# Performance work log

Hardware: AMD Instinct MI355X
Metric: run time of the kernel (lower is better)

## Reference

```python
import jax, jax.numpy as jnp
import numpy as np

LOG2PI = float(np.log(2.0 * np.pi))


def setup_inputs() -> dict:
    key = jax.random.key(0)
    ks = jax.random.split(key, 5)
    B, T, XD, C = 128, 2050, 6, 64
    return {
        "x": jax.random.normal(ks[0], (B, T, XD), jnp.float32),
        "observation_means": jax.random.uniform(ks[1], (C, XD), dtype=jnp.float32),
        "observation_stddevs": jax.random.uniform(ks[2], (C, XD), dtype=jnp.float32),
        "log_A": jax.random.normal(ks[3], (C, C), jnp.float32),
        "log_pi": jax.random.normal(ks[4], (C,), jnp.float32),
    }


def _emission_logprob(x, means, stds):
    # Normal(means[:, :4], relu(stds[:, :4]) + 0.1).log_prob(x[:, :, :4]) summed over feat dim
    mu = means[:, :4]                       # (C,4)
    sigma = jax.nn.relu(stds[:, :4]) + 0.1  # (C,4)
    z = (x[:, :, None, :4] - mu) / sigma    # (B,T,C,4)
    return jnp.sum(-0.5 * z * z - jnp.log(sigma) - 0.5 * LOG2PI, axis=-1)  # (B,T,C)


def _forward_scalers(logp, log_A, log_pi):
    # scaled HMM forward pass; returns per-step log normalizers (T,B)
    a0 = logp[:, 0] + log_pi
    s0 = jax.nn.logsumexp(a0, axis=-1)
    a0n = a0 - s0[:, None]

    def step(a_prev, lp_t):
        a = lp_t + jax.nn.logsumexp(a_prev[:, :, None] + log_A[None], axis=1)
        s = jax.nn.logsumexp(a, axis=-1)
        return a - s[:, None], s

    _, s_rest = jax.lax.scan(step, a0n, jnp.swapaxes(logp[:, 1:], 0, 1))
    return jnp.concatenate([s0[None], s_rest], axis=0)  # (T,B)


def _viterbi(logp, log_A, log_pi):
    d0 = logp[:, 0] + log_pi  # (B,C)

    def step(d_prev, lp_t):
        scores = d_prev[:, :, None] + log_A[None]  # (B,C_prev,C_cur)
        psi_t = jnp.argmax(scores, axis=1)
        d = jnp.max(scores, axis=1) + lp_t
        return d, psi_t

    d_last, psi = jax.lax.scan(step, d0, jnp.swapaxes(logp[:, 1:], 0, 1))  # psi: (T-1,B,C)
    c_last = jnp.argmax(d_last, axis=-1)  # (B,)

    def back(c_next, psi_t):
        c_t = jnp.take_along_axis(psi_t, c_next[:, None], axis=1)[:, 0]
        return c_t, c_t

    _, cs = jax.lax.scan(back, c_last, psi, reverse=True)  # (T-1,B)
    c = jnp.concatenate([cs, c_last[None]], axis=0)  # (T,B)
    return jnp.swapaxes(c, 0, 1)  # (B,T)


def reference(x, observation_means, observation_stddevs, log_A, log_pi):
    logA = jax.nn.log_softmax(log_A, axis=1)
    logpi = jax.nn.log_softmax(log_pi, axis=0)
    logp = _emission_logprob(x, observation_means, observation_stddevs)  # (B,T,C)
    scalers = _forward_scalers(logp, logA, logpi)                         # (T,B)
    logp_x = jnp.sum(scalers, axis=0)                                     # (B,)
    c_est = _viterbi(logp, logA, logpi)                                   # (B,T) int
    return logp_x, c_est
```

## Files before the change

### kernel.cpp

```cpp
#include <hip/hip_runtime.h>

#define T_LEN 2050
#define B_SZ 128
#define NCHUNK 33
#define HL2PI 0.91893853320467274178f

__device__ __forceinline__ float waveMax(float v) {
#pragma unroll
    for (int off = 32; off >= 1; off >>= 1)
        v = fmaxf(v, __shfl_xor(v, off, 64));
    return v;
}
__device__ __forceinline__ float waveSum(float v) {
#pragma unroll
    for (int off = 32; off >= 1; off >>= 1)
        v += __shfl_xor(v, off, 64);
    return v;
}
__device__ __forceinline__ void waveArgmax(float& v, int& idx) {
#pragma unroll
    for (int off = 32; off >= 1; off >>= 1) {
        float ov = __shfl_xor(v, off, 64);
        int   oi = __shfl_xor(idx, off, 64);
        if (ov > v || (ov == v && oi < idx)) { v = ov; idx = oi; }
    }
}
__device__ __forceinline__ void cfence() { asm volatile("" ::: "memory"); }

__device__ __forceinline__ float rl(float v, int lane) {
    return __int_as_float(__builtin_amdgcn_readlane(__float_as_int(v), lane));
}

__device__ __forceinline__ float dppSumAll(float v) {
#define SSTEP(ctrl) { int t_ = __builtin_amdgcn_update_dpp(0, __float_as_int(v), ctrl, 0xf, 0xf, true); \
                      v = v + __int_as_float(t_); }
    SSTEP(0x111) SSTEP(0x112) SSTEP(0x114) SSTEP(0x118) SSTEP(0x142) SSTEP(0x143)
#undef SSTEP
    return __int_as_float(__builtin_amdgcn_readlane(__float_as_int(v), 63));
}
__device__ __forceinline__ float dppMaxAll(float v) {
#define MSTEP(ctrl) { int t_ = __builtin_amdgcn_update_dpp(__float_as_int(v), __float_as_int(v), ctrl, 0xf, 0xf, false); \
                      v = fmaxf(v, __int_as_float(t_)); }
    MSTEP(0x111) MSTEP(0x112) MSTEP(0x114) MSTEP(0x118) MSTEP(0x142) MSTEP(0x143)
#undef MSTEP
    return __int_as_float(__builtin_amdgcn_readlane(__float_as_int(v), 63));
}

extern "C" __global__ __launch_bounds__(64, 1)
void hmm_prep(const float* __restrict__ logA_in,
              const float* __restrict__ logpi_in,
              float* __restrict__ lAg,
              float* __restrict__ lpig)
{
    __shared__ float la[64 * 65];
    __shared__ float rowlse[64];
    const int j = threadIdx.x;
#pragma unroll
    for (int k = 0; k < 64; ++k)
        la[k * 65 + j] = logA_in[k * 64 + j];
    cfence();
    {
        float m = -1e30f;
#pragma unroll
        for (int k = 0; k < 64; ++k) m = fmaxf(m, la[j * 65 + k]);
        float s = 0.f;
#pragma unroll
        for (int k = 0; k < 64; ++k) s += expf(la[j * 65 + k] - m);
        rowlse[j] = m + logf(s);
    }
    cfence();
    {
        float v = logpi_in[j];
        float m = waveMax(v);
        float s = waveSum(expf(v - m));
        lpig[j] = v - (m + logf(s));
    }
    float4* o = (float4*)lAg;
#pragma unroll
    for (int k = 0; k < 16; ++k) {
        float4 v;
        v.x = la[(4 * k + 0) * 65 + j] - rowlse[4 * k + 0];
        v.y = la[(4 * k + 1) * 65 + j] - rowlse[4 * k + 1];
        v.z = la[(4 * k + 2) * 65 + j] - rowlse[4 * k + 2];
        v.w = la[(4 * k + 3) * 65 + j] - rowlse[4 * k + 3];
        o[j * 16 + k] = v;
    }
}

extern "C" __global__ __launch_bounds__(256)
void hmm_emis(const float* __restrict__ x,
              const float* __restrict__ means,
              const float* __restrict__ stds,
              float* __restrict__ buf,
              float* __restrict__ m_pre)
{
    const int wid = blockIdx.x * 4 + (threadIdx.x >> 6);
    const int j = threadIdx.x & 63;
    const int t = wid >> 7;
    const int b = wid & 127;

    const float* xt = x + ((size_t)b * T_LEN + t) * 6;
    float x0 = xt[0], x1 = xt[1], x2 = xt[2], x3 = xt[3];

    float mu0 = means[j * 6 + 0], mu1 = means[j * 6 + 1];
    float mu2 = means[j * 6 + 2], mu3 = means[j * 6 + 3];
    float sg0 = fmaxf(stds[j * 6 + 0], 0.f) + 0.1f;
    float sg1 = fmaxf(stds[j * 6 + 1], 0.f) + 0.1f;
    float sg2 = fmaxf(stds[j * 6 + 2], 0.f) + 0.1f;
    float sg3 = fmaxf(stds[j * 6 + 3], 0.f) + 0.1f;
    float ls0 = logf(sg0), ls1 = logf(sg1), ls2 = logf(sg2), ls3 = logf(sg3);

    float z0 = (x0 - mu0) / sg0, z1 = (x1 - mu1) / sg1;
    float z2 = (x2 - mu2) / sg2, z3 = (x3 - mu3) / sg3;
    float e0 = ((-0.5f * z0) * z0 - ls0) - HL2PI;
    float e1 = ((-0.5f * z1) * z1 - ls1) - HL2PI;
    float e2 = ((-0.5f * z2) * z2 - ls2) - HL2PI;
    float e3 = ((-0.5f * z3) * z3 - ls3) - HL2PI;
    float lp = ((e0 + e1) + e2) + e3;

    buf[((size_t)b * T_LEN + t) * 64 + j] = lp;
    float mm = waveMax(lp);
    if (j == 0) m_pre[(size_t)b * T_LEN + t] = mm;
}

#define VIT_REDUCE(SRC)                                                   \
    float m0 = -3.4e38f, m1 = -3.4e38f, m2 = -3.4e38f, m3 = -3.4e38f;     \
    _Pragma("unroll")                                                     \
    for (int gq = 0; gq < 4; ++gq) {                                      \
        float s_[16];                                                     \
        _Pragma("unroll")                                                 \
        for (int m_ = 0; m_ < 16; ++m_) s_[m_] = rl((SRC), 16 * gq + m_); \
        __builtin_amdgcn_sched_barrier(0);                                \
        _Pragma("unroll")                                                 \
        for (int k2 = 0; k2 < 4; k2 += 2) {                               \
            const int ia = 16 * gq + 4 * k2;                              \
            const int ib = ia + 4;                                        \
            float a0_ = s_[4*k2+0] + lA[ia+0], b0_ = s_[4*k2+4] + lA[ib+0]; \
            float a1_ = s_[4*k2+1] + lA[ia+1], b1_ = s_[4*k2+5] + lA[ib+1]; \
            float a2_ = s_[4*k2+2] + lA[ia+2], b2_ = s_[4*k2+6] + lA[ib+2]; \
            float a3_ = s_[4*k2+3] + lA[ia+3], b3_ = s_[4*k2+7] + lA[ib+3]; \
            m0 = fmaxf(fmaxf(m0, a0_), b0_);                              \
            m1 = fmaxf(fmaxf(m1, a1_), b1_);                              \
            m2 = fmaxf(fmaxf(m2, a2_), b2_);                              \
            m3 = fmaxf(fmaxf(m3, a3_), b3_);                              \
        }                                                                 \
    }

extern "C" __global__ __launch_bounds__(64, 1)
void hmm_main(const float* __restrict__ x,
              const float* __restrict__ means,
              const float* __restrict__ stds,
              const float* __restrict__ lAg,
              const float* __restrict__ lpig,
              float* __restrict__ out,
              float* __restrict__ buf,
              const float* __restrict__ m_pre,
              int* __restrict__ c_last)
{
    __shared__ __align__(16) float xs[12304];

    const int j   = threadIdx.x;
    const int bid = blockIdx.x;
    const bool is_fwd = (bid < B_SZ);
    const int b = is_fwd ? bid : bid - B_SZ;

    float lpi = lpig[j];

    if (is_fwd) {
        {
            const float4* xg4 = (const float4*)(x + (size_t)b * T_LEN * 6);
            float4* xs4 = (float4*)xs;
            for (int i = j; i < 3075; i += 64) xs4[i] = xg4[i];
        }
        float mu0 = means[j * 6 + 0], mu1 = means[j * 6 + 1];
        float mu2 = means[j * 6 + 2], mu3 = means[j * 6 + 3];
        float sg0 = fmaxf(stds[j * 6 + 0], 0.f) + 0.1f;
        float sg1 = fmaxf(stds[j * 6 + 1], 0.f) + 0.1f;
        float sg2 = fmaxf(stds[j * 6 + 2], 0.f) + 0.1f;
        float sg3 = fmaxf(stds[j * 6 + 3], 0.f) + 0.1f;
        float ls0 = logf(sg0), ls1 = logf(sg1), ls2 = logf(sg2), ls3 = logf(sg3);
        float i0 = 1.f / sg0, i1 = 1.f / sg1, i2 = 1.f / sg2, i3 = 1.f / sg3;
        float cst = -(ls0 + ls1 + ls2 + ls3) - 4.f * HL2PI;

        float Ac[64];
        {
            const float4* g = (const float4*)lAg;
#pragma unroll
            for (int k = 0; k < 16; ++k) {
                float4 v = g[j * 16 + k];
                Ac[4 * k + 0] = __expf(v.x); Ac[4 * k + 1] = __expf(v.y);
                Ac[4 * k + 2] = __expf(v.z); Ac[4 * k + 3] = __expf(v.w);
            }
        }
        cfence();

        float z0 = (xs[0] - mu0) * i0, z1 = (xs[1] - mu1) * i1;
        float z2 = (xs[2] - mu2) * i2, z3 = (xs[3] - mu3) * i3;
        float a0 = (cst - 0.5f * (z0 * z0 + z1 * z1 + z2 * z2 + z3 * z3)) + lpi;
        float m0a = dppMaxAll(a0);
        float u = __expf(a0 - m0a);
        float s0 = dppSumAll(u);
        double acc = (double)(m0a + __logf(s0));
        u *= (1.0f / s0);

        const float* mp = m_pre + (size_t)b * T_LEN;
        float g0 = mp[1], g1 = mp[2], g2 = mp[3], g3 = mp[4];

#pragma unroll 1
        for (int t = 1; t < T_LEN; ++t) {
            float mm_c = g0; g0 = g1; g1 = g2; g2 = g3;
            int tp = t + 4; if (tp > T_LEN - 1) tp = T_LEN - 1;
            g3 = mp[tp];

            int o = t * 6;
            float y0 = xs[o], y1 = xs[o + 1], y2 = xs[o + 2], y3 = xs[o + 3];
            float w0 = (y0 - mu0) * i0, w1 = (y1 - mu1) * i1;
            float w2 = (y2 - mu2) * i2, w3 = (y3 - mu3) * i3;
            float lp = cst - 0.5f * (w0 * w0 + w1 * w1 + w2 * w2 + w3 * w3);
            float e_c = __expf(lp - mm_c);

            float q0 = 0.f, q1 = 0.f, q2 = 0.f, q3 = 0.f;
#pragma unroll
            for (int gq = 0; gq < 4; ++gq) {
                float s[16];
#pragma unroll
                for (int m = 0; m < 16; ++m) s[m] = rl(u, 16 * gq + m);
#pragma unroll
                for (int k2 = 0; k2 < 4; ++k2) {
                    const int i = 16 * gq + 4 * k2;
                    q0 = fmaf(s[4 * k2 + 0], Ac[i + 0], q0);
                    q1 = fmaf(s[4 * k2 + 1], Ac[i + 1], q1);
                    q2 = fmaf(s[4 * k2 + 2], Ac[i + 2], q2);
                    q3 = fmaf(s[4 * k2 + 3], Ac[i + 3], q3);
                }
            }
            u = ((q0 + q1) + (q2 + q3)) * e_c;
            acc += (double)mm_c;
            if ((t & 3) == 0) {
                float ss = dppSumAll(u);
                acc += (double)__logf(ss);
                u *= (1.0f / ss);
            }
        }
        float sf = dppSumAll(u);
        acc += (double)__logf(sf);
        if (j == 0) out[b] = (float)acc;
    } else {
        float lA[64];
        {
            const float4* g = (const float4*)lAg;
#pragma unroll
            for (int k = 0; k < 16; ++k) {
                float4 v = g[j * 16 + k];
                lA[4 * k + 0] = v.x; lA[4 * k + 1] = v.y;
                lA[4 * k + 2] = v.z; lA[4 * k + 3] = v.w;
            }
        }
        float* bb = buf + (size_t)b * T_LEN * 64 + j;

        float dn = bb[0] + lpi;
        float lr[8];
#pragma unroll
        for (int i = 0; i < 8; ++i) lr[i] = bb[(size_t)(1 + i) * 64];
        bb[0] = dn;

#pragma unroll 1
        for (int tb = 1; tb <= 2033; tb += 8) {
#pragma unroll
            for (int q = 0; q < 8; ++q) {
                const int t = tb + q;
                float lp_c = lr[q];
                lr[q] = bb[(size_t)(t + 8) * 64];
                VIT_REDUCE(dn);
                dn = fmaxf(fmaxf(m0, m1), fmaxf(m2, m3)) + lp_c;
                bb[(size_t)t * 64] = dn;
            }
        }
        float l_last = bb[(size_t)2049 * 64];
#pragma unroll
        for (int q = 0; q < 8; ++q) {
            const int t = 2041 + q;
            float lp_c = lr[q];
            VIT_REDUCE(dn);
            dn = fmaxf(fmaxf(m0, m1), fmaxf(m2, m3)) + lp_c;
            bb[(size_t)t * 64] = dn;
        }
        {
            float lp_c = l_last;
            VIT_REDUCE(dn);
            dn = fmaxf(fmaxf(m0, m1), fmaxf(m2, m3)) + lp_c;
        }

        float vv = dn; int idx = j;
        waveArgmax(vv, idx);
        if (j == 0) c_last[b] = idx;
    }
}

extern "C" __global__ __launch_bounds__(256)
void hmm_psi(const float* __restrict__ buf,
             const float* __restrict__ lAg,
             unsigned char* __restrict__ psi)
{
    __shared__ __align__(16) float sd[4][64];
    const int warp = threadIdx.x >> 6;
    const int j = threadIdx.x & 63;
    const int wid = blockIdx.x * 4 + warp;

    float lA[64];
    {
        const float4* g = (const float4*)lAg;
#pragma unroll
        for (int k = 0; k < 16; ++k) {
            float4 v = g[j * 16 + k];
            lA[4 * k + 0] = v.x; lA[4 * k + 1] = v.y;
            lA[4 * k + 2] = v.z; lA[4 * k + 3] = v.w;
        }
    }
    const float4* dv = (const float4*)sd[warp];
    const int NP = 2049 * B_SZ;

    for (int p = wid; p < NP; p += 8192) {
        const int t = (p >> 7) + 1;
        const int b = p & 127;
        float dval = buf[((size_t)b * T_LEN + (t - 1)) * 64 + j];
        sd[warp][j] = dval;

        float bv0 = -3.4e38f, bv1 = -3.4e38f, bv2 = -3.4e38f, bv3 = -3.4e38f;
        int bi0 = 0, bi1 = 1, bi2 = 2, bi3 = 3;
#pragma unroll
        for (int k = 0; k < 16; ++k) {
            float4 dd = dv[k];
            float v0 = dd.x + lA[4 * k + 0];
            float v1 = dd.y + lA[4 * k + 1];
            float v2 = dd.z + lA[4 * k + 2];
            float v3 = dd.w + lA[4 * k + 3];
            if (v0 > bv0) { bv0 = v0; bi0 = 4 * k + 0; }
            if (v1 > bv1) { bv1 = v1; bi1 = 4 * k + 1; }
            if (v2 > bv2) { bv2 = v2; bi2 = 4 * k + 2; }
            if (v3 > bv3) { bv3 = v3; bi3 = 4 * k + 3; }
        }
        float best = bv0; int bidx = bi0;
        if (bv1 > best || (bv1 == best && bi1 < bidx)) { best = bv1; bidx = bi1; }
        if (bv2 > best || (bv2 == best && bi2 < bidx)) { best = bv2; bidx = bi2; }
        if (bv3 > best || (bv3 == best && bi3 < bidx)) { best = bv3; bidx = bi3; }

        psi[((size_t)t * B_SZ + b) * 64 + j] = (unsigned char)bidx;
    }
}

extern "C" __global__ __launch_bounds__(256)
void hmm_compose(const unsigned char* __restrict__ psi,
                 unsigned char* __restrict__ mt)
{
    const int w = blockIdx.x * 4 + (threadIdx.x >> 6);
    const int j = threadIdx.x & 63;
    const int g = w % NCHUNK;
    const int b = w / NCHUNK;
    const int e  = (g < NCHUNK - 1) ? g * 64 + 64 : (T_LEN - 1);
    const int t0 = g * 64 + 1;

    int M = j;
    int r[8];
#pragma unroll
    for (int i = 0; i < 8; ++i) {
        int t = e - i;
        r[i] = (t >= t0) ? (int)psi[((size_t)t * B_SZ + b) * 64 + j] : 0;
    }
#pragma unroll 1
    for (int t = e; t >= t0; --t) {
        const int q = (e - t) & 7;
        int row = r[q];
        int tn = t - 8;
        r[q] = (tn >= t0) ? (int)psi[((size_t)tn * B_SZ + b) * 64 + j] : 0;
        M = __builtin_amdgcn_ds_bpermute(M << 2, row);
    }
    mt[((size_t)g * B_SZ + b) * 64 + j] = (unsigned char)M;
}

extern "C" __global__ __launch_bounds__(64, 1)
void hmm_bound(const unsigned char* __restrict__ mt,
               const int* __restrict__ c_last,
               int* __restrict__ sbg)
{
    const int b = blockIdx.x;
    const int j = threadIdx.x;
    int rows[NCHUNK];
#pragma unroll
    for (int q = 0; q < NCHUNK; ++q)
        rows[q] = (int)mt[((size_t)q * B_SZ + b) * 64 + j];
    int cur = c_last[b];
#pragma unroll
    for (int q = NCHUNK - 1; q >= 0; --q) {
        cur = __builtin_amdgcn_readlane(rows[q], cur);
        if (j == 0) sbg[b * NCHUNK + q] = cur;
    }
}

extern "C" __global__ __launch_bounds__(256)
void hmm_fill(const unsigned char* __restrict__ psi,
              const int* __restrict__ sbg,
              const int* __restrict__ c_last,
              float* __restrict__ out)
{
    const int w = blockIdx.x * 4 + (threadIdx.x >> 6);
    const int j = threadIdx.x & 63;
    const int g = w % NCHUNK;
    const int b = w / NCHUNK;
    const int cl = c_last[b];
    float* oc = out + B_SZ + (size_t)b * T_LEN;

    const int e  = (g < NCHUNK - 1) ? g * 64 + 64 : (T_LEN - 1);
    const int t0 = g * 64 + 1;
    int s = (g < NCHUNK - 1) ? sbg[b * NCHUNK + g + 1] : cl;
    if (g == NCHUNK - 1 && j == 0) oc[T_LEN - 1] = (float)cl;

    int r[8];
#pragma unroll
    for (int i = 0; i < 8; ++i) {
        int t = e - i;
        r[i] = (t >= t0) ? (int)psi[((size_t)t * B_SZ + b) * 64 + j] : 0;
    }
#pragma unroll 1
    for (int t = e; t >= t0; --t) {
        const int q = (e - t) & 7;
        int row = r[q];
        int tn = t - 8;
        r[q] = (tn >= t0) ? (int)psi[((size_t)tn * B_SZ + b) * 64 + j] : 0;
        s = __builtin_amdgcn_readlane(row, s);
        if (j == 0) oc[t - 1] = (float)s;
    }
}

extern "C" void kernel_launch(void* const* d_in, const int* in_sizes, int n_in,
                              void* d_out, int out_size, void* d_ws, size_t ws_size,
                              hipStream_t stream)
{
    const float* x      = (const float*)d_in[0];
    const float* means  = (const float*)d_in[1];
    const float* stds   = (const float*)d_in[2];
    const float* logA   = (const float*)d_in[3];
    const float* logpi  = (const float*)d_in[4];
    float* out = (float*)d_out;

    char* base = (char*)d_ws;
    float*         buf   = (float*)base;
    unsigned char* psi   = (unsigned char*)(base + 67174400);
    float*         m_pre = (float*)(base + 67174400);
    unsigned char* mt    = (unsigned char*)(base + 83968000);
    int*           cl    = (int*)(base + 84238336);
    float*         lAg   = (float*)(base + 84238848);
    float*         lpig  = (float*)(base + 84255232);
    int*           sbg   = (int*)base;

    hipLaunchKernelGGL(hmm_prep, dim3(1), dim3(64), 0, stream, logA, logpi, lAg, lpig);
    hipLaunchKernelGGL(hmm_emis, dim3((T_LEN * B_SZ) / 4), dim3(256), 0, stream,
                       x, means, stds, buf, m_pre);
    hipLaunchKernelGGL(hmm_main, dim3(2 * B_SZ), dim3(64), 0, stream,
                       x, means, stds, lAg, lpig, out, buf, m_pre, cl);
    hipLaunchKernelGGL(hmm_psi, dim3(2048), dim3(256), 0, stream, buf, lAg, psi);
    hipLaunchKernelGGL(hmm_compose, dim3((NCHUNK * B_SZ) / 4), dim3(256), 0, stream, psi, mt);
    hipLaunchKernelGGL(hmm_bound, dim3(B_SZ), dim3(64), 0, stream, mt, cl, sbg);
    hipLaunchKernelGGL(hmm_fill, dim3((NCHUNK * B_SZ) / 4), dim3(256), 0, stream, psi, sbg, cl, out);
}
```

Measured before the change: 1.018 ms.

## Fuse prep into emission kernel and merge backtrace stages into cooperative kernel

Folds the logA/logpi normalisation into block 0 of the emission kernel, and merges the psi, compose, bound and fill kernels into one cooperative kernel with grid.sync between stages. The aim is to remove several kernel launches and their inter-launch gaps. In exchange, the psi stage now runs on 768 blocks instead of 2048, and cooperative launch plus grid-wide barriers add their own costs. Moving prep into emis is safe because emis does not read lAg and hmm_main runs after emis.

```diff
diff --git a/kernel.cpp b/kernel.cpp
--- a/kernel.cpp
+++ b/kernel.cpp
@@ -1,4 +1,7 @@
 #include <hip/hip_runtime.h>
+#include <hip/hip_cooperative_groups.h>
+
+namespace cg = cooperative_groups;
 
 #define T_LEN 2050
 #define B_SZ 128
@@ -46,54 +49,20 @@
     return __int_as_float(__builtin_amdgcn_readlane(__float_as_int(v), 63));
 }
 
-extern "C" __global__ __launch_bounds__(64, 1)
-void hmm_prep(const float* __restrict__ logA_in,
+extern "C" __global__ __launch_bounds__(256)
+void hmm_emis(const float* __restrict__ x,
+              const float* __restrict__ means,
+              const float* __restrict__ stds,
+              float* __restrict__ buf,
+              float* __restrict__ m_pre,
+              const float* __restrict__ logA_in,
               const float* __restrict__ logpi_in,
               float* __restrict__ lAg,
               float* __restrict__ lpig)
 {
     __shared__ float la[64 * 65];
     __shared__ float rowlse[64];
-    const int j = threadIdx.x;
-#pragma unroll
-    for (int k = 0; k < 64; ++k)
-        la[k * 65 + j] = logA_in[k * 64 + j];
-    cfence();
-    {
-        float m = -1e30f;
-#pragma unroll
-        for (int k = 0; k < 64; ++k) m = fmaxf(m, la[j * 65 + k]);
-        float s = 0.f;
-#pragma unroll
-        for (int k = 0; k < 64; ++k) s += expf(la[j * 65 + k] - m);
-        rowlse[j] = m + logf(s);
-    }
-    cfence();
-    {
-        float v = logpi_in[j];
-        float m = waveMax(v);
-        float s = waveSum(expf(v - m));
-        lpig[j] = v - (m + logf(s));
-    }
-    float4* o = (float4*)lAg;
-#pragma unroll
-    for (int k = 0; k < 16; ++k) {
-        float4 v;
-        v.x = la[(4 * k + 0) * 65 + j] - rowlse[4 * k + 0];
-        v.y = la[(4 * k + 1) * 65 + j] - rowlse[4 * k + 1];
-        v.z = la[(4 * k + 2) * 65 + j] - rowlse[4 * k + 2];
-        v.w = la[(4 * k + 3) * 65 + j] - rowlse[4 * k + 3];
-        o[j * 16 + k] = v;
-    }
-}
-
-extern "C" __global__ __launch_bounds__(256)
-void hmm_emis(const float* __restrict__ x,
-              const float* __restrict__ means,
-              const float* __restrict__ stds,
-              float* __restrict__ buf,
-              float* __restrict__ m_pre)
-{
+
     const int wid = blockIdx.x * 4 + (threadIdx.x >> 6);
     const int j = threadIdx.x & 63;
     const int t = wid >> 7;
@@ -121,6 +90,39 @@
     buf[((size_t)b * T_LEN + t) * 64 + j] = lp;
     float mm = waveMax(lp);
     if (j == 0) m_pre[(size_t)b * T_LEN + t] = mm;
+
+    if (blockIdx.x == 0 && threadIdx.x < 64) {
+#pragma unroll
+        for (int k = 0; k < 64; ++k)
+            la[k * 65 + j] = logA_in[k * 64 + j];
+        cfence();
+        {
+            float m = -1e30f;
+#pragma unroll
+            for (int k = 0; k < 64; ++k) m = fmaxf(m, la[j * 65 + k]);
+            float s = 0.f;
+#pragma unroll
+            for (int k = 0; k < 64; ++k) s += expf(la[j * 65 + k] - m);
+            rowlse[j] = m + logf(s);
+        }
+        cfence();
+        {
+            float v = logpi_in[j];
+            float m = waveMax(v);
+            float s = waveSum(expf(v - m));
+            lpig[j] = v - (m + logf(s));
+        }
+        float4* o = (float4*)lAg;
+#pragma unroll
+        for (int k = 0; k < 16; ++k) {
+            float4 v;
+            v.x = la[(4 * k + 0) * 65 + j] - rowlse[4 * k + 0];
+            v.y = la[(4 * k + 1) * 65 + j] - rowlse[4 * k + 1];
+            v.z = la[(4 * k + 2) * 65 + j] - rowlse[4 * k + 2];
+            v.w = la[(4 * k + 3) * 65 + j] - rowlse[4 * k + 3];
+            o[j * 16 + k] = v;
+        }
+    }
 }
 
 #define VIT_REDUCE(SRC)                                                   \
@@ -298,137 +300,130 @@
 }
 
 extern "C" __global__ __launch_bounds__(256)
-void hmm_psi(const float* __restrict__ buf,
-             const float* __restrict__ lAg,
-             unsigned char* __restrict__ psi)
+void hmm_back(const float* __restrict__ buf,
+              const float* __restrict__ lAg,
+              unsigned char* __restrict__ psi,
+              unsigned char* __restrict__ mt,
+              const int* __restrict__ c_last,
+              int* __restrict__ sbg,
+              float* __restrict__ out)
 {
+    cg::grid_group grid = cg::this_grid();
     __shared__ __align__(16) float sd[4][64];
     const int warp = threadIdx.x >> 6;
     const int j = threadIdx.x & 63;
     const int wid = blockIdx.x * 4 + warp;
-
-    float lA[64];
+    const int NW = 768 * 4;
+
     {
-        const float4* g = (const float4*)lAg;
-#pragma unroll
-        for (int k = 0; k < 16; ++k) {
-            float4 v = g[j * 16 + k];
-            lA[4 * k + 0] = v.x; lA[4 * k + 1] = v.y;
-            lA[4 * k + 2] = v.z; lA[4 * k + 3] = v.w;
-        }
-    }
-    const float4* dv = (const float4*)sd[warp];
-    const int NP = 2049 * B_SZ;
-
-    for (int p = wid; p < NP; p += 8192) {
-        const int t = (p >> 7) + 1;
-        const int b = p & 127;
-        float dval = buf[((size_t)b * T_LEN + (t - 1)) * 64 + j];
-        sd[warp][j] = dval;
-
-        float bv0 = -3.4e38f, bv1 = -3.4e38f, bv2 = -3.4e38f, bv3 = -3.4e38f;
-        int bi0 = 0, bi1 = 1, bi2 = 2, bi3 = 3;
-#pragma unroll
-        for (int k = 0; k < 16; ++k) {
-            float4 dd = dv[k];
-            float v0 = dd.x + lA[4 * k + 0];
-            float v1 = dd.y + lA[4 * k + 1];
-            float v2 = dd.z + lA[4 * k + 2];
-            float v3 = dd.w + lA[4 * k + 3];
-            if (v0 > bv0) { bv0 = v0; bi0 = 4 * k + 0; }
-            if (v1 > bv1) { bv1 = v1; bi1 = 4 * k + 1; }
-            if (v2 > bv2) { bv2 = v2; bi2 = 4 * k + 2; }
-            if (v3 > bv3) { bv3 = v3; bi3 = 4 * k + 3; }
-        }
-        float best = bv0; int bidx = bi0;
-        if (bv1 > best || (bv1 == best && bi1 < bidx)) { best = bv1; bidx = bi1; }
-        if (bv2 > best || (bv2 == best && bi2 < bidx)) { best = bv2; bidx = bi2; }
-        if (bv3 > best || (bv3 == best && bi3 < bidx)) { best = bv3; bidx = bi3; }
-
-        psi[((size_t)t * B_SZ + b) * 64 + j] = (unsigned char)bidx;
-    }
-}
-
-extern "C" __global__ __launch_bounds__(256)
-void hmm_compose(const unsigned char* __restrict__ psi,
-                 unsigned char* __restrict__ mt)
-{
-    const int w = blockIdx.x * 4 + (threadIdx.x >> 6);
-    const int j = threadIdx.x & 63;
-    const int g = w % NCHUNK;
-    const int b = w / NCHUNK;
-    const int e  = (g < NCHUNK - 1) ? g * 64 + 64 : (T_LEN - 1);
-    const int t0 = g * 64 + 1;
-
-    int M = j;
-    int r[8];
-#pragma unroll
-    for (int i = 0; i < 8; ++i) {
-        int t = e - i;
-        r[i] = (t >= t0) ? (int)psi[((size_t)t * B_SZ + b) * 64 + j] : 0;
-    }
+        float lA[64];
+        {
+            const float4* g = (const float4*)lAg;
+#pragma unroll
+            for (int k = 0; k < 16; ++k) {
+                float4 v = g[j * 16 + k];
+                lA[4 * k + 0] = v.x; lA[4 * k + 1] = v.y;
+                lA[4 * k + 2] = v.z; lA[4 * k + 3] = v.w;
+            }
+        }
+        const float4* dv = (const float4*)sd[warp];
+        const int NP = 2049 * B_SZ;
+        for (int p = wid; p < NP; p += NW) {
+            const int t = (p >> 7) + 1;
+            const int b = p & 127;
+            float dval = buf[((size_t)b * T_LEN + (t - 1)) * 64 + j];
+            sd[warp][j] = dval;
+
+            float bv0 = -3.4e38f, bv1 = -3.4e38f, bv2 = -3.4e38f, bv3 = -3.4e38f;
+            int bi0 = 0, bi1 = 1, bi2 = 2, bi3 = 3;
+#pragma unroll
+            for (int k = 0; k < 16; ++k) {
+                float4 dd = dv[k];
+                float v0 = dd.x + lA[4 * k + 0];
+                float v1 = dd.y + lA[4 * k + 1];
+                float v2 = dd.z + lA[4 * k + 2];
+                float v3 = dd.w + lA[4 * k + 3];
+                if (v0 > bv0) { bv0 = v0; bi0 = 4 * k + 0; }
+                if (v1 > bv1) { bv1 = v1; bi1 = 4 * k + 1; }
+                if (v2 > bv2) { bv2 = v2; bi2 = 4 * k + 2; }
+                if (v3 > bv3) { bv3 = v3; bi3 = 4 * k + 3; }
+            }
+            float best = bv0; int bidx = bi0;
+            if (bv1 > best || (bv1 == best && bi1 < bidx)) { best = bv1; bidx = bi1; }
+            if (bv2 > best || (bv2 == best && bi2 < bidx)) { best = bv2; bidx = bi2; }
+            if (bv3 > best || (bv3 == best && bi3 < bidx)) { best = bv3; bidx = bi3; }
+
+            psi[((size_t)t * B_SZ + b) * 64 + j] = (unsigned char)bidx;
+        }
+    }
+    grid.sync();
+
+    for (int w = wid; w < NCHUNK * B_SZ; w += NW) {
+        const int g = w % NCHUNK;
+        const int b = w / NCHUNK;
+        const int e  = (g < NCHUNK - 1) ? g * 64 + 64 : (T_LEN - 1);
+        const int t0 = g * 64 + 1;
+
+        int M = j;
+        int r[8];
+#pragma unroll
+        for (int i = 0; i < 8; ++i) {
+            int t = e - i;
+            r[i] = (t >= t0) ? (int)psi[((size_t)t * B_SZ + b) * 64 + j] : 0;
+        }
 #pragma unroll 1
-    for (int t = e; t >= t0; --t) {
-        const int q = (e - t) & 7;
-        int row = r[q];
-        int tn = t - 8;
-        r[q] = (tn >= t0) ? (int)psi[((size_t)tn * B_SZ + b) * 64 + j] : 0;
-        M = __builtin_amdgcn_ds_bpermute(M << 2, row);
-    }
-    mt[((size_t)g * B_SZ + b) * 64 + j] = (unsigned char)M;
-}
-
-extern "C" __global__ __launch_bounds__(64, 1)
-void hmm_bound(const unsigned char* __restrict__ mt,
-               const int* __restrict__ c_last,
-               int* __restrict__ sbg)
-{
-    const int b = blockIdx.x;
-    const int j = threadIdx.x;
-    int rows[NCHUNK];
-#pragma unroll
-    for (int q = 0; q < NCHUNK; ++q)
-        rows[q] = (int)mt[((size_t)q * B_SZ + b) * 64 + j];
-    int cur = c_last[b];
-#pragma unroll
-    for (int q = NCHUNK - 1; q >= 0; --q) {
-        cur = __builtin_amdgcn_readlane(rows[q], cur);
-        if (j == 0) sbg[b * NCHUNK + q] = cur;
-    }
-}
-
-extern "C" __global__ __launch_bounds__(256)
-void hmm_fill(const unsigned char* __restrict__ psi,
-              const int* __restrict__ sbg,
-              const int* __restrict__ c_last,
-              float* __restrict__ out)
-{
-    const int w = blockIdx.x * 4 + (threadIdx.x >> 6);
-    const int j = threadIdx.x & 63;
-    const int g = w % NCHUNK;
-    const int b = w / NCHUNK;
-    const int cl = c_last[b];
-    float* oc = out + B_SZ + (size_t)b * T_LEN;
-
-    const int e  = (g < NCHUNK - 1) ? g * 64 + 64 : (T_LEN - 1);
-    const int t0 = g * 64 + 1;
-    int s = (g < NCHUNK - 1) ? sbg[b * NCHUNK + g + 1] : cl;
-    if (g == NCHUNK - 1 && j == 0) oc[T_LEN - 1] = (float)cl;
-
-    int r[8];
-#pragma unroll
-    for (int i = 0; i < 8; ++i) {
-        int t = e - i;
-        r[i] = (t >= t0) ? (int)psi[((size_t)t * B_SZ + b) * 64 + j] : 0;
-    }
+        for (int t = e; t >= t0; --t) {
+            const int q = (e - t) & 7;
+            int row = r[q];
+            int tn = t - 8;
+            r[q] = (tn >= t0) ? (int)psi[((size_t)tn * B_SZ + b) * 64 + j] : 0;
+            M = __builtin_amdgcn_ds_bpermute(M << 2, row);
+        }
+        mt[((size_t)g * B_SZ + b) * 64 + j] = (unsigned char)M;
+    }
+    grid.sync();
+
+    if (wid < B_SZ) {
+        const int b = wid;
+        int rows[NCHUNK];
+#pragma unroll
+        for (int q = 0; q < NCHUNK; ++q)
+            rows[q] = (int)mt[((size_t)q * B_SZ + b) * 64 + j];
+        int cur = c_last[b];
+#pragma unroll
+        for (int q = NCHUNK - 1; q >= 0; --q) {
+            cur = __builtin_amdgcn_readlane(rows[q], cur);
+            if (j == 0) sbg[b * NCHUNK + q] = cur;
+        }
+    }
+    grid.sync();
+
+    for (int w = wid; w < NCHUNK * B_SZ; w += NW) {
+        const int g = w % NCHUNK;
+        const int b = w / NCHUNK;
+        const int cl = c_last[b];
+        float* oc = out + B_SZ + (size_t)b * T_LEN;
+
+        const int e  = (g < NCHUNK - 1) ? g * 64 + 64 : (T_LEN - 1);
+        const int t0 = g * 64 + 1;
+        int s = (g < NCHUNK - 1) ? sbg[b * NCHUNK + g + 1] : cl;
+        if (g == NCHUNK - 1 && j == 0) oc[T_LEN - 1] = (float)cl;
+
+        int r[8];
+#pragma unroll
+        for (int i = 0; i < 8; ++i) {
+            int t = e - i;
+            r[i] = (t >= t0) ? (int)psi[((size_t)t * B_SZ + b) * 64 + j] : 0;
+        }
 #pragma unroll 1
-    for (int t = e; t >= t0; --t) {
-        const int q = (e - t) & 7;
-        int row = r[q];
-        int tn = t - 8;
-        r[q] = (tn >= t0) ? (int)psi[((size_t)tn * B_SZ + b) * 64 + j] : 0;
-        s = __builtin_amdgcn_readlane(row, s);
-        if (j == 0) oc[t - 1] = (float)s;
+        for (int t = e; t >= t0; --t) {
+            const int q = (e - t) & 7;
+            int row = r[q];
+            int tn = t - 8;
+            r[q] = (tn >= t0) ? (int)psi[((size_t)tn * B_SZ + b) * 64 + j] : 0;
+            s = __builtin_amdgcn_readlane(row, s);
+            if (j == 0) oc[t - 1] = (float)s;
+        }
     }
 }
 
@@ -453,13 +448,14 @@
     float*         lpig  = (float*)(base + 84255232);
     int*           sbg   = (int*)base;
 
-    hipLaunchKernelGGL(hmm_prep, dim3(1), dim3(64), 0, stream, logA, logpi, lAg, lpig);
     hipLaunchKernelGGL(hmm_emis, dim3((T_LEN * B_SZ) / 4), dim3(256), 0, stream,
-                       x, means, stds, buf, m_pre);
+                       x, means, stds, buf, m_pre, logA, logpi, lAg, lpig);
     hipLaunchKernelGGL(hmm_main, dim3(2 * B_SZ), dim3(64), 0, stream,
                        x, means, stds, lAg, lpig, out, buf, m_pre, cl);
-    hipLaunchKernelGGL(hmm_psi, dim3(2048), dim3(256), 0, stream, buf, lAg, psi);
-    hipLaunchKernelGGL(hmm_compose, dim3((NCHUNK * B_SZ) / 4), dim3(256), 0, stream, psi, mt);
-    hipLaunchKernelGGL(hmm_bound, dim3(B_SZ), dim3(64), 0, stream, mt, cl, sbg);
-    hipLaunchKernelGGL(hmm_fill, dim3((NCHUNK * B_SZ) / 4), dim3(256), 0, stream, psi, sbg, cl, out);
-}
+    {
+        void* bargs[] = { (void*)&buf, (void*)&lAg, (void*)&psi, (void*)&mt,
+                          (void*)&cl, (void*)&sbg, (void*)&out };
+        hipLaunchCooperativeKernel((void*)hmm_back, dim3(768), dim3(256),
+                                   bargs, 0, stream);
+    }
+}
```

After: 1.272 ms. 24.9% more time.
